# Performance work log

Measured on AMD Instinct MI355X. Metric: run time of the kernel, lower is better.

Reference implementation:

```python
import jax, jax.numpy as jnp
import numpy as np
from jax import lax

# 4D spatial convolution dimension numbers: batch, channel, 4 spatial axes (X,Y,Z,W)
DN = ('NCXYZW', 'OIXYZW', 'NCXYZW')


def setup_inputs() -> dict:
    key = jax.random.key(0)
    k1, k2, k3, k4, k5 = jax.random.split(key, 5)
    B, S, K = 512, 18, 13
    x = jax.random.normal(k1, (B, 1, S, S, S, S), dtype=jnp.float32)
    # conv4d(1, 3, 13): weight [out=3, in=1, 13,13,13,13], torch-style init scale
    fan_in = 1 * K ** 4
    conv_w = jax.random.normal(k2, (3, 1, K, K, K, K), dtype=jnp.float32) / np.sqrt(fan_in)
    conv_b = jax.random.normal(k3, (3,), dtype=jnp.float32) * 0.01
    # Linear(3 * 6**4 = 3888, 1)
    lin_w = jax.random.normal(k4, (1, 3888), dtype=jnp.float32) / np.sqrt(3888)
    lin_b = jax.random.normal(k5, (1,), dtype=jnp.float32) * 0.01
    return {'x': x, 'conv_w': conv_w, 'conv_b': conv_b, 'lin_w': lin_w, 'lin_b': lin_b}


def reference(x, conv_w, conv_b, lin_w, lin_b):
    # 4D conv (cross-correlation, matching torch), VALID padding, stride 1
    h = lax.conv_general_dilated(
        x, conv_w,
        window_strides=(1, 1, 1, 1),
        padding='VALID',
        dimension_numbers=DN,
    )  # [B, 3, 6, 6, 6, 6]
    h = h + conv_b[None, :, None, None, None, None]
    h = jax.nn.relu(h)
    # Flatten (channel-major, same as torch.flatten) -> [B, 3888]
    h = h.reshape(h.shape[0], -1)
    # Dropout(0.5) is identity in eval mode. Linear + Sigmoid.
    logits = h @ lin_w.T + lin_b  # [B, 1]
    return jax.nn.sigmoid(logits)
```

## Files before the change

kernel.cpp:

```cpp
#include <hip/hip_runtime.h>

typedef unsigned short u16;
typedef __bf16 v8bf __attribute__((ext_vector_type(8)));
typedef float v4f __attribute__((ext_vector_type(4)));
typedef u16 v8u16 __attribute__((ext_vector_type(8)));

#define X_B 104976
#define X_A 5832
#define X_P 324
#define XB_B 106272
#define XB_A 5904
#define XB_P 328
#define XB_ELEMS 54411328u
#define KP 59488
#define SLAB 352
#define NPAD 112
#define B2_ELEMS 6662656u
#define C_ELEMS 2064384u
#define WS_C   0
#define WS_B2  8257536ull
#define WS_XB  21582848ull
#define WS_FAST_NEED 130405504ull

__device__ __forceinline__ u16 f2bf(float f) {
    unsigned u = __builtin_bit_cast(unsigned, f);
    u += 0x7fffu + ((u >> 16) & 1u);
    return (u16)(u >> 16);
}

#define AS1C(p) (const __attribute__((address_space(1))) void*)(p)
#define AS3(p)  (__attribute__((address_space(3))) void*)(p)

__global__ void conv_bf16_kernel(const float* __restrict__ X, u16* __restrict__ Xb) {
    unsigned gid = blockIdx.x * 256u + threadIdx.x;
    if (gid >= XB_ELEMS) return;
    unsigned plane = gid / 328u;
    unsigned pos = gid - plane * 328u;
    u16 v = 0;
    if (plane < 165888u && pos < 324u)
        v = f2bf(X[plane * 324u + pos]);
    Xb[gid] = v;
}

__global__ void build_b2_kernel(const float* __restrict__ W, u16* __restrict__ B2,
                                float* __restrict__ C) {
    unsigned idx = blockIdx.x * 256u + threadIdx.x;
    if (idx < C_ELEMS) C[idx] = 0.f;
    if (idx >= B2_ELEMS) return;
    unsigned n = idx / (unsigned)KP;
    unsigned k = idx - n * (unsigned)KP;
    u16 v = 0;
    if (n < 108u) {
        unsigned slab = k / 352u;
        unsigned jj = k - slab * 352u;
        if (jj < 324u) {
            unsigned kx = slab / 13u, ky = slab - kx * 13u;
            unsigned jz = jj / 18u, jw = jj - jz * 18u;
            unsigned o = n / 36u, zw = n - o * 36u;
            unsigned zo = zw / 6u, wo = zw - zo * 6u;
            int dz = (int)jz - (int)zo, dw = (int)jw - (int)wo;
            if (dz >= 0 && dz < 13 && dw >= 0 && dw < 13)
                v = f2bf(W[o * 28561u + kx * 2197u + ky * 169u + (unsigned)dz * 13u + (unsigned)dw]);
        }
    }
    B2[idx] = v;
}

template<bool USE_XB>
__global__ __launch_bounds__(256, 2) void gemm_conv(
    const u16* __restrict__ Xb, const float* __restrict__ Xf,
    const u16* __restrict__ B2, float* __restrict__ C)
{
    __shared__ u16 Alds[256 * 32];
    __shared__ u16 Blds[112 * 32];

    const int tid = threadIdx.x;
    const int lane = tid & 63;
    const int wv = tid >> 6;
    const int mt = blockIdx.x % 72;
    const int ks = blockIdx.x / 72;

    const int sbeg = (ks * 169) / 7;
    const int send = ((ks + 1) * 169) / 7;
    const int nsteps = (send - sbeg) * 11;

    int laneA[4], chunkA[4];
#pragma unroll
    for (int jr = 0; jr < 4; ++jr) {
        int slot = jr * 256 + tid;
        int row = slot >> 2;
        int chunk = slot & 3;
        int r = mt * 256 + row;
        int b = r / 36;
        int xy = r - b * 36;
        int x = xy / 6;
        int y = xy - x * 6;
        if (USE_XB) laneA[jr] = b * XB_B + x * XB_A + y * XB_P + chunk * 8;
        else        laneA[jr] = b * X_B + x * X_A + y * X_P;
        chunkA[jr] = chunk;
    }
    const int laneB0 = (tid >> 2) * KP + (tid & 3) * 8;
    const int laneB1 = laneB0 + 64 * KP;

    v4f acc[4][7];
#pragma unroll
    for (int i = 0; i < 4; ++i)
#pragma unroll
        for (int t = 0; t < 7; ++t) acc[i][t] = (v4f){0.f, 0.f, 0.f, 0.f};

    for (int step = 0; step < nsteps; ++step) {
        int q = step / 11;
        int si = step - q * 11;
        int slab = sbeg + q;
        int kx = slab / 13;
        int ky = slab - kx * 13;

        if (USE_XB) {
            int aofs = kx * XB_A + ky * XB_P + si * 32;
#pragma unroll
            for (int jr = 0; jr < 4; ++jr) {
                const u16* gp = Xb + (laneA[jr] + aofs);
                __builtin_amdgcn_global_load_lds(AS1C(gp), AS3(&Alds[(jr * 256 + wv * 64) * 8]), 16, 0, 0);
            }
        } else {
            int aofs = kx * X_A + ky * X_P;
#pragma unroll
            for (int jr = 0; jr < 4; ++jr) {
                int jj0 = si * 32 + chunkA[jr] * 8;
                const float* gp = Xf + (laneA[jr] + aofs);
                float4 lo = make_float4(0.f, 0.f, 0.f, 0.f);
                float4 hi = make_float4(0.f, 0.f, 0.f, 0.f);
                if (jj0 < 324)     lo = *(const float4*)(gp + jj0);
                if (jj0 + 4 < 324) hi = *(const float4*)(gp + jj0 + 4);
                v8u16 p;
                p[0] = f2bf(lo.x); p[1] = f2bf(lo.y); p[2] = f2bf(lo.z); p[3] = f2bf(lo.w);
                p[4] = f2bf(hi.x); p[5] = f2bf(hi.y); p[6] = f2bf(hi.z); p[7] = f2bf(hi.w);
                int slot = jr * 256 + tid;
                *(v8u16*)(&Alds[slot * 8]) = p;
            }
        }
        {
            int bofs = slab * SLAB + si * 32;
            const u16* gp0 = B2 + (laneB0 + bofs);
            __builtin_amdgcn_global_load_lds(AS1C(gp0), AS3(&Blds[(wv * 64) * 8]), 16, 0, 0);
            if (wv < 3) {
                const u16* gp1 = B2 + (laneB1 + bofs);
                __builtin_amdgcn_global_load_lds(AS1C(gp1), AS3(&Blds[(256 + wv * 64) * 8]), 16, 0, 0);
            }
        }
        __syncthreads();

        v8bf a[4];
#pragma unroll
        for (int i = 0; i < 4; ++i)
            a[i] = *(const v8bf*)(&Alds[(wv * 64 + i * 16 + (lane & 15)) * 32 + (lane >> 4) * 8]);
#pragma unroll
        for (int t = 0; t < 7; ++t) {
            v8bf bb = *(const v8bf*)(&Blds[(t * 16 + (lane & 15)) * 32 + (lane >> 4) * 8]);
#pragma unroll
            for (int i = 0; i < 4; ++i)
                acc[i][t] = __builtin_amdgcn_mfma_f32_16x16x32_bf16(a[i], bb, acc[i][t], 0, 0, 0);
        }
        __syncthreads();
    }

    const int colb = lane & 15;
    const int rq = (lane >> 4) * 4;
#pragma unroll
    for (int i = 0; i < 4; ++i) {
        int rowb = mt * 256 + wv * 64 + i * 16 + rq;
#pragma unroll
        for (int t = 0; t < 7; ++t) {
            int col = t * 16 + colb;
#pragma unroll
            for (int g = 0; g < 4; ++g)
                atomicAdd(&C[(rowb + g) * NPAD + col], acc[i][t][g]);
        }
    }
}

__global__ void epilogue_kernel(const float* __restrict__ C, const float* __restrict__ cb,
                                const float* __restrict__ lw, const float* __restrict__ lb,
                                float* __restrict__ out) {
    const int b = blockIdx.x;
    const int tid = threadIdx.x;
    float s = 0.f;
    for (int t = tid; t < 3888; t += 256) {
        int xy = t / 108, n = t - xy * 108;
        int o = n / 36, zw = n - o * 36;
        int x = xy / 6, y = xy - x * 6;
        float c = C[(b * 36 + xy) * NPAD + n] + cb[o];
        s += fmaxf(c, 0.f) * lw[o * 1296 + x * 216 + y * 36 + zw];
    }
#pragma unroll
    for (int off = 32; off > 0; off >>= 1) s += __shfl_down(s, off, 64);
    __shared__ float red[4];
    if ((tid & 63) == 0) red[tid >> 6] = s;
    __syncthreads();
    if (tid == 0)
        out[b] = 1.f / (1.f + expf(-(red[0] + red[1] + red[2] + red[3] + lb[0])));
}

extern "C" void kernel_launch(void* const* d_in, const int* in_sizes, int n_in,
                              void* d_out, int out_size, void* d_ws, size_t ws_size,
                              hipStream_t stream) {
    const float* X  = (const float*)d_in[0];
    const float* W  = (const float*)d_in[1];
    const float* cb = (const float*)d_in[2];
    const float* lw = (const float*)d_in[3];
    const float* lb = (const float*)d_in[4];
    float* out = (float*)d_out;
    char* ws = (char*)d_ws;
    float* C  = (float*)(ws + WS_C);
    u16* B2   = (u16*)(ws + WS_B2);
    u16* Xb   = (u16*)(ws + WS_XB);
    const bool fast = ws_size >= WS_FAST_NEED;

    build_b2_kernel<<<26026, 256, 0, stream>>>(W, B2, C);
    if (fast) {
        conv_bf16_kernel<<<(XB_ELEMS + 255) / 256, 256, 0, stream>>>(X, Xb);
        gemm_conv<true><<<504, 256, 0, stream>>>(Xb, X, B2, C);
    } else {
        gemm_conv<false><<<504, 256, 0, stream>>>(nullptr, X, B2, C);
    }
    epilogue_kernel<<<512, 256, 0, stream>>>(C, cb, lw, lb, out);
}
```

Measured before the change: 760.2 us.

## Double-buffer LDS in conv GEMM, swizzle LDS layout, vectorize prep kernels

Splits the GEMM main loop into a prefetch stage that writes the next K-step into a second LDS buffer while MFMAs consume the current one, leaving one barrier per step. It adds an XOR swizzle on the 16-byte chunk index for the A and B tiles to reduce LDS bank conflicts on fragment reads. The bf16 conversion and B2 build kernels are rewritten to process eight elements per thread with vector loads and stores. This doubles LDS use, which could affect occupancy at two blocks per CU.

```diff
diff --git a/kernel.cpp b/kernel.cpp
--- a/kernel.cpp
+++ b/kernel.cpp
@@ -32,38 +32,50 @@
 #define AS3(p)  (__attribute__((address_space(3))) void*)(p)
 
 __global__ void conv_bf16_kernel(const float* __restrict__ X, u16* __restrict__ Xb) {
-    unsigned gid = blockIdx.x * 256u + threadIdx.x;
-    if (gid >= XB_ELEMS) return;
-    unsigned plane = gid / 328u;
-    unsigned pos = gid - plane * 328u;
-    u16 v = 0;
-    if (plane < 165888u && pos < 324u)
-        v = f2bf(X[plane * 324u + pos]);
-    Xb[gid] = v;
+    const int bx = blockIdx.x;
+    const long xbbase = (long)bx * XB_A;
+    const long xfbase = (long)bx * X_A;
+    for (int s = threadIdx.x; s < 738; s += 256) {
+        int y = s / 41;
+        int pos = (s - y * 41) * 8;
+        const float* src = X + xfbase + y * 324 + pos;
+        float4 lo = *(const float4*)src;
+        float4 hi = (pos + 4 < 324) ? *(const float4*)(src + 4)
+                                    : make_float4(0.f, 0.f, 0.f, 0.f);
+        v8u16 p;
+        p[0] = f2bf(lo.x); p[1] = f2bf(lo.y); p[2] = f2bf(lo.z); p[3] = f2bf(lo.w);
+        p[4] = f2bf(hi.x); p[5] = f2bf(hi.y); p[6] = f2bf(hi.z); p[7] = f2bf(hi.w);
+        *(v8u16*)(Xb + xbbase + s * 8) = p;
+    }
 }
 
 __global__ void build_b2_kernel(const float* __restrict__ W, u16* __restrict__ B2,
                                 float* __restrict__ C) {
-    unsigned idx = blockIdx.x * 256u + threadIdx.x;
-    if (idx < C_ELEMS) C[idx] = 0.f;
-    if (idx >= B2_ELEMS) return;
-    unsigned n = idx / (unsigned)KP;
-    unsigned k = idx - n * (unsigned)KP;
-    u16 v = 0;
-    if (n < 108u) {
-        unsigned slab = k / 352u;
-        unsigned jj = k - slab * 352u;
-        if (jj < 324u) {
-            unsigned kx = slab / 13u, ky = slab - kx * 13u;
-            unsigned jz = jj / 18u, jw = jj - jz * 18u;
-            unsigned o = n / 36u, zw = n - o * 36u;
-            unsigned zo = zw / 6u, wo = zw - zo * 6u;
-            int dz = (int)jz - (int)zo, dw = (int)jw - (int)wo;
-            if (dz >= 0 && dz < 13 && dw >= 0 && dw < 13)
-                v = f2bf(W[o * 28561u + kx * 2197u + ky * 169u + (unsigned)dz * 13u + (unsigned)dw]);
-        }
-    }
-    B2[idx] = v;
+    unsigned t = blockIdx.x * 256u + threadIdx.x;
+    if (t < 516096u) ((float4*)C)[t] = make_float4(0.f, 0.f, 0.f, 0.f);
+    if (t >= 832832u) return;
+    unsigned n = t / 7436u;
+    unsigned k0 = (t - n * 7436u) * 8u;
+    unsigned slab = k0 / 352u;
+    unsigned jj0 = k0 - slab * 352u;
+    v8u16 out = {0, 0, 0, 0, 0, 0, 0, 0};
+    if (n < 108u && jj0 < 324u) {
+        unsigned kx = slab / 13u, ky = slab - kx * 13u;
+        unsigned o = n / 36u, zw = n - o * 36u;
+        unsigned zo = zw / 6u, wo = zw - zo * 6u;
+        const float* wb = W + o * 28561u + kx * 2197u + ky * 169u;
+#pragma unroll
+        for (int e = 0; e < 8; ++e) {
+            unsigned jj = jj0 + e;
+            if (jj < 324u) {
+                unsigned jz = jj / 18u, jw = jj - jz * 18u;
+                int dz = (int)jz - (int)zo, dw = (int)jw - (int)wo;
+                if (dz >= 0 && dz < 13 && dw >= 0 && dw < 13)
+                    out[e] = f2bf(wb[dz * 13 + dw]);
+            }
+        }
+    }
+    ((v8u16*)B2)[t] = out;
 }
 
 template<bool USE_XB>
@@ -71,8 +83,8 @@
     const u16* __restrict__ Xb, const float* __restrict__ Xf,
     const u16* __restrict__ B2, float* __restrict__ C)
 {
-    __shared__ u16 Alds[256 * 32];
-    __shared__ u16 Blds[112 * 32];
+    __shared__ u16 Alds[2][256 * 32];
+    __shared__ u16 Blds[2][112 * 32];
 
     const int tid = threadIdx.x;
     const int lane = tid & 63;
@@ -89,7 +101,7 @@
     for (int jr = 0; jr < 4; ++jr) {
         int slot = jr * 256 + tid;
         int row = slot >> 2;
-        int chunk = slot & 3;
+        int chunk = (slot & 3) ^ ((slot >> 3) & 3);
         int r = mt * 256 + row;
         int b = r / 36;
         int xy = r - b * 36;
@@ -99,7 +111,8 @@
         else        laneA[jr] = b * X_B + x * X_A + y * X_P;
         chunkA[jr] = chunk;
     }
-    const int laneB0 = (tid >> 2) * KP + (tid & 3) * 8;
+    const int chunkB = (tid & 3) ^ ((tid >> 3) & 3);
+    const int laneB0 = (tid >> 2) * KP + chunkB * 8;
     const int laneB1 = laneB0 + 64 * KP;
 
     v4f acc[4][7];
@@ -108,19 +121,18 @@
 #pragma unroll
         for (int t = 0; t < 7; ++t) acc[i][t] = (v4f){0.f, 0.f, 0.f, 0.f};
 
-    for (int step = 0; step < nsteps; ++step) {
+    auto stage = [&](int step, int p) {
         int q = step / 11;
         int si = step - q * 11;
         int slab = sbeg + q;
         int kx = slab / 13;
         int ky = slab - kx * 13;
-
         if (USE_XB) {
             int aofs = kx * XB_A + ky * XB_P + si * 32;
 #pragma unroll
             for (int jr = 0; jr < 4; ++jr) {
                 const u16* gp = Xb + (laneA[jr] + aofs);
-                __builtin_amdgcn_global_load_lds(AS1C(gp), AS3(&Alds[(jr * 256 + wv * 64) * 8]), 16, 0, 0);
+                __builtin_amdgcn_global_load_lds(AS1C(gp), AS3(&Alds[p][(jr * 256 + wv * 64) * 8]), 16, 0, 0);
             }
         } else {
             int aofs = kx * X_A + ky * X_P;
@@ -132,36 +144,46 @@
                 float4 hi = make_float4(0.f, 0.f, 0.f, 0.f);
                 if (jj0 < 324)     lo = *(const float4*)(gp + jj0);
                 if (jj0 + 4 < 324) hi = *(const float4*)(gp + jj0 + 4);
-                v8u16 p;
-                p[0] = f2bf(lo.x); p[1] = f2bf(lo.y); p[2] = f2bf(lo.z); p[3] = f2bf(lo.w);
-                p[4] = f2bf(hi.x); p[5] = f2bf(hi.y); p[6] = f2bf(hi.z); p[7] = f2bf(hi.w);
+                v8u16 pk;
+                pk[0] = f2bf(lo.x); pk[1] = f2bf(lo.y); pk[2] = f2bf(lo.z); pk[3] = f2bf(lo.w);
+                pk[4] = f2bf(hi.x); pk[5] = f2bf(hi.y); pk[6] = f2bf(hi.z); pk[7] = f2bf(hi.w);
                 int slot = jr * 256 + tid;
-                *(v8u16*)(&Alds[slot * 8]) = p;
+                *(v8u16*)(&Alds[p][slot * 8]) = pk;
             }
         }
-        {
-            int bofs = slab * SLAB + si * 32;
-            const u16* gp0 = B2 + (laneB0 + bofs);
-            __builtin_amdgcn_global_load_lds(AS1C(gp0), AS3(&Blds[(wv * 64) * 8]), 16, 0, 0);
-            if (wv < 3) {
-                const u16* gp1 = B2 + (laneB1 + bofs);
-                __builtin_amdgcn_global_load_lds(AS1C(gp1), AS3(&Blds[(256 + wv * 64) * 8]), 16, 0, 0);
-            }
-        }
-        __syncthreads();
+        int bofs = slab * SLAB + si * 32;
+        const u16* gp0 = B2 + (laneB0 + bofs);
+        __builtin_amdgcn_global_load_lds(AS1C(gp0), AS3(&Blds[p][(wv * 64) * 8]), 16, 0, 0);
+        if (wv < 3) {
+            const u16* gp1 = B2 + (laneB1 + bofs);
+            __builtin_amdgcn_global_load_lds(AS1C(gp1), AS3(&Blds[p][(256 + wv * 64) * 8]), 16, 0, 0);
+        }
+    };
+
+    stage(0, 0);
+
+    for (int step = 0; step < nsteps; ++step) {
+        const int p = step & 1;
+        __builtin_amdgcn_s_waitcnt(0);
+        __builtin_amdgcn_s_barrier();
+        if (step + 1 < nsteps) stage(step + 1, p ^ 1);
 
         v8bf a[4];
 #pragma unroll
-        for (int i = 0; i < 4; ++i)
-            a[i] = *(const v8bf*)(&Alds[(wv * 64 + i * 16 + (lane & 15)) * 32 + (lane >> 4) * 8]);
+        for (int i = 0; i < 4; ++i) {
+            int row = wv * 64 + i * 16 + (lane & 15);
+            int slot = row * 4 + ((lane >> 4) ^ ((row >> 1) & 3));
+            a[i] = *(const v8bf*)(&Alds[p][slot * 8]);
+        }
 #pragma unroll
         for (int t = 0; t < 7; ++t) {
-            v8bf bb = *(const v8bf*)(&Blds[(t * 16 + (lane & 15)) * 32 + (lane >> 4) * 8]);
+            int row = t * 16 + (lane & 15);
+            int slot = row * 4 + ((lane >> 4) ^ ((row >> 1) & 3));
+            v8bf bb = *(const v8bf*)(&Blds[p][slot * 8]);
 #pragma unroll
             for (int i = 0; i < 4; ++i)
                 acc[i][t] = __builtin_amdgcn_mfma_f32_16x16x32_bf16(a[i], bb, acc[i][t], 0, 0, 0);
         }
-        __syncthreads();
     }
 
     const int colb = lane & 15;
@@ -216,9 +238,9 @@
     u16* Xb   = (u16*)(ws + WS_XB);
     const bool fast = ws_size >= WS_FAST_NEED;
 
-    build_b2_kernel<<<26026, 256, 0, stream>>>(W, B2, C);
+    build_b2_kernel<<<3254, 256, 0, stream>>>(W, B2, C);
     if (fast) {
-        conv_bf16_kernel<<<(XB_ELEMS + 255) / 256, 256, 0, stream>>>(X, Xb);
+        conv_bf16_kernel<<<9216, 256, 0, stream>>>(X, Xb);
         gemm_conv<true><<<504, 256, 0, stream>>>(Xb, X, B2, C);
     } else {
         gemm_conv<false><<<504, 256, 0, stream>>>(nullptr, X, B2, C);
```

New measurement: 733.4 us. 1.04x faster.
